# Kernel tuning notes

Hardware: AMD Instinct MI355X
Metric: run time of the kernel (lower is better)

The kernel has to match this reference:

```python
import jax, jax.numpy as jnp
import numpy as np

N_NODES = 50000
N_EDGES = 800000
D_IN = 128
D_HID = 128
N_CLASSES = 40


def gcn_conv(h, src, dst, W, b, n_nodes):
    """GCNConv: out = D^{-1/2} (A + I) D^{-1/2} (h @ W) + b, with self-loops."""
    h = h @ W  # [N, F_out]
    loop = jnp.arange(n_nodes, dtype=src.dtype)
    s = jnp.concatenate([src, loop])  # [E + N]
    d = jnp.concatenate([dst, loop])
    deg = jax.ops.segment_sum(jnp.ones_like(d, dtype=h.dtype), d, num_segments=n_nodes)
    dinv = jax.lax.rsqrt(jnp.maximum(deg, 1.0))  # deg >= 1 due to self-loops
    norm = dinv[s] * dinv[d]  # [E + N]
    msgs = h[s] * norm[:, None]  # gather: [E + N, F_out]
    out = jax.ops.segment_sum(msgs, d, num_segments=n_nodes)  # scatter-add
    return out + b


def setup_inputs() -> dict:
    key = jax.random.key(0)
    ks = jax.random.split(key, 12)
    x = jax.random.normal(ks[0], (N_NODES, D_IN), dtype=jnp.float32)
    edge_index = jax.random.randint(ks[1], (2, N_EDGES), 0, N_NODES, dtype=jnp.int64)
    def lin(k, fi, fo):
        s = 1.0 / np.sqrt(fi)
        return jax.random.uniform(k, (fi, fo), jnp.float32, -s, s)
    W_pre = lin(ks[2], D_IN, D_HID)
    b_pre = jnp.zeros((D_HID,), jnp.float32)
    W1 = lin(ks[3], D_HID, D_HID)
    b1 = jnp.zeros((D_HID,), jnp.float32)
    W2 = lin(ks[4], D_HID, D_HID)
    b2 = jnp.zeros((D_HID,), jnp.float32)
    W_post = lin(ks[5], D_HID, N_CLASSES)
    b_post = jnp.zeros((N_CLASSES,), jnp.float32)
    return {"x": x, "edge_index": edge_index, "W_pre": W_pre, "b_pre": b_pre,
            "W1": W1, "b1": b1, "W2": W2, "b2": b2,
            "W_post": W_post, "b_post": b_post}


def reference(x, edge_index, W_pre, b_pre, W1, b1, W2, b2, W_post, b_post):
    src, dst = edge_index[0], edge_index[1]
    n = x.shape[0]
    h = x @ W_pre + b_pre                      # pre-process MLP (Linear)
    h = jax.nn.relu(gcn_conv(h, src, dst, W1, b1, n))   # conv1 + act1
    h = jax.nn.relu(gcn_conv(h, src, dst, W2, b2, n))   # conv2 + act2
    return h @ W_post + b_post                 # post-process MLP (Linear)
```

## Files before the change

kernel.cpp:

```cpp
#include <hip/hip_runtime.h>

#define D 128

typedef short bfrag __attribute__((ext_vector_type(8)));
typedef float f32x4 __attribute__((ext_vector_type(4)));
typedef unsigned uint32;

__device__ inline unsigned short bf16_rne(float x) {
    unsigned u = __float_as_uint(x);
    return (unsigned short)((u + 0x7FFFu + ((u >> 16) & 1u)) >> 16);
}
__device__ inline float bf16_to_f(unsigned short h) {
    return __uint_as_float(((unsigned)h) << 16);
}
__device__ inline unsigned split2p(float x) {
    unsigned short hi = bf16_rne(x);
    unsigned short lo = bf16_rne(x - bf16_to_f(hi));
    return (unsigned)hi | ((unsigned)lo << 16);
}

__device__ inline void unpair_r(uint4 q0, uint4 q1, bfrag& ah, bfrag& al) {
    union { uint32 u[4]; bfrag b; } H, L;
    H.u[0] = __builtin_amdgcn_perm(q0.y, q0.x, 0x05040100u);
    H.u[1] = __builtin_amdgcn_perm(q0.w, q0.z, 0x05040100u);
    H.u[2] = __builtin_amdgcn_perm(q1.y, q1.x, 0x05040100u);
    H.u[3] = __builtin_amdgcn_perm(q1.w, q1.z, 0x05040100u);
    L.u[0] = __builtin_amdgcn_perm(q0.y, q0.x, 0x07060302u);
    L.u[1] = __builtin_amdgcn_perm(q0.w, q0.z, 0x07060302u);
    L.u[2] = __builtin_amdgcn_perm(q1.y, q1.x, 0x07060302u);
    L.u[3] = __builtin_amdgcn_perm(q1.w, q1.z, 0x07060302u);
    ah = H.b;
    al = L.b;
}

__device__ inline void split8_r(uint4 q0, uint4 q1, bfrag& ah, bfrag& al) {
    float v[8] = {__uint_as_float(q0.x), __uint_as_float(q0.y), __uint_as_float(q0.z), __uint_as_float(q0.w),
                  __uint_as_float(q1.x), __uint_as_float(q1.y), __uint_as_float(q1.z), __uint_as_float(q1.w)};
    union { unsigned short us[8]; bfrag b; } H, L;
    #pragma unroll
    for (int i = 0; i < 8; i++) {
        unsigned pr = split2p(v[i]);
        H.us[i] = (unsigned short)pr;
        L.us[i] = (unsigned short)(pr >> 16);
    }
    ah = H.b;
    al = L.b;
}

__global__ __launch_bounds__(256) void compose_w(const float* __restrict__ Wpre, const float* __restrict__ W1,
                                                 const float* __restrict__ bpre,
                                                 uint32* __restrict__ wcp, float* __restrict__ bc) {
    int gid = blockIdx.x * 256 + threadIdx.x;
    int i = gid >> 2;
    int kq = gid & 3;
    int n = i & 127, k = i >> 7;
    float acc = 0.f;
    #pragma unroll 8
    for (int m = kq * 32; m < kq * 32 + 32; m++)
        acc = fmaf(Wpre[k * 128 + m], W1[m * 128 + n], acc);
    acc += __shfl_xor(acc, 1);
    acc += __shfl_xor(acc, 2);
    if (kq == 0) {
        wcp[n * 128 + k] = split2p(acc);
        if (i < 128) {
            float b = 0.f;
            #pragma unroll 8
            for (int m = 0; m < 128; m++)
                b = fmaf(bpre[m], W1[m * 128 + i], b);
            bc[i] = b;
        }
    }
}

__global__ __launch_bounds__(256) void deg_raw(const unsigned* __restrict__ raw, int* __restrict__ deg,
                                               unsigned* __restrict__ e32, unsigned short* __restrict__ csr16,
                                               float* __restrict__ t_c, int E, int Npad, int csrCap4, int nRows,
                                               const float* __restrict__ W2, const float* __restrict__ Wpost,
                                               uint32* __restrict__ w2_p, uint32* __restrict__ wpost_p) {
    __shared__ int smode;
    int gid = blockIdx.x * 256 + threadIdx.x;
    int gstride = gridDim.x * 256;
    int p0 = blockIdx.x * 1024;
    if (threadIdx.x < 64) {
        int p = p0 + threadIdx.x * 16;
        unsigned v = (p < E) ? raw[2 * p + 1] : 0u;
        unsigned long long any = __ballot(v != 0u);
        if (threadIdx.x == 0) smode = (any != 0ull) ? 1 : 0;
    }
    __syncthreads();
    int m = smode;
    unsigned short sent = (unsigned short)Npad;
    ushort4 s4 = make_ushort4(sent, sent, sent, sent);
    for (int i = gid; i < csrCap4; i += gstride) ((ushort4*)csr16)[i] = s4;
    int sentRows = nRows - Npad;
    int nSentF4 = 8 * sentRows * 4;
    for (int i = gid; i < nSentF4; i += gstride) {
        int chunk = i / (sentRows * 4);
        int rem = i % (sentRows * 4);
        ((float4*)(t_c + (size_t)chunk * nRows * 16 + (size_t)Npad * 16))[rem] = make_float4(0.f, 0.f, 0.f, 0.f);
    }
    for (int i = gid; i < 22528; i += gstride) {
        const float* W; uint32* wp; int idx, ncols;
        if (i < 16384) { W = W2;    wp = w2_p;    idx = i;         ncols = 128; }
        else           { W = Wpost; wp = wpost_p; idx = i - 16384; ncols = 40;  }
        int n = idx >> 7, k = idx & 127;
        float v = (n < ncols) ? W[k * ncols + n] : 0.f;
        wp[idx] = split2p(v);
    }
    int pend = min(p0 + 1024, E);
    for (int p = p0 + threadIdx.x; p < pend; p += 256) {
        int s, d;
        if (m) { s = (int)raw[p]; d = (int)raw[E + p]; }
        else   { s = (int)((const unsigned long long*)raw)[p]; d = (int)((const unsigned long long*)raw)[E + p]; }
        e32[p] = (unsigned)s | ((unsigned)d << 16);
        atomicAdd(&deg[d], 1);
    }
}

__global__ __launch_bounds__(256) void rank_block(const int* __restrict__ deg, float* __restrict__ dinv,
                                                  int* __restrict__ local_rank, int* __restrict__ hist_blk, int N) {
    __shared__ int h[256];
    int t = threadIdx.x;
    h[t] = 0;
    __syncthreads();
    int i = blockIdx.x * 256 + t;
    if (i < N) {
        int d = deg[i];
        dinv[i] = 1.0f / sqrtf((float)(d + 1));
        int b = min(d, 255);
        local_rank[i] = atomicAdd(&h[b], 1);
    }
    __syncthreads();
    hist_blk[blockIdx.x * 256 + t] = h[t];
}

__global__ __launch_bounds__(256) void scan_blocks(int* __restrict__ hist_blk, int* __restrict__ binbase,
                                                   int* __restrict__ ebase, int nblk) {
    int b = threadIdx.x;
    int sum = 0;
    int k = 0;
    for (; k + 8 <= nblk; k += 8) {
        int v[8];
        #pragma unroll
        for (int u = 0; u < 8; u++) v[u] = hist_blk[(k + u) * 256 + b];
        #pragma unroll
        for (int u = 0; u < 8; u++) { hist_blk[(k + u) * 256 + b] = sum; sum += v[u]; }
    }
    for (; k < nblk; k++) {
        int v = hist_blk[k * 256 + b];
        hist_blk[k * 256 + b] = sum;
        sum += v;
    }
    __shared__ int s[256], s2[256];
    int bp = (b + 3) & ~3;
    int c = sum, e = sum * bp;
    s[b] = c; s2[b] = e;
    __syncthreads();
    for (int off = 1; off < 256; off <<= 1) {
        int a0 = (b >= off) ? s[b - off] : 0;
        int a1 = (b >= off) ? s2[b - off] : 0;
        __syncthreads();
        s[b] += a0; s2[b] += a1;
        __syncthreads();
    }
    binbase[b] = s[b] - c;
    ebase[b] = s2[b] - e;
}

__global__ __launch_bounds__(256) void emit_perm(const int* __restrict__ deg, const float* __restrict__ dinv,
                                                 const int* __restrict__ local_rank, const int* __restrict__ hist_blk,
                                                 const int* __restrict__ binbase, const int* __restrict__ ebase,
                                                 int* __restrict__ tailcur, int* __restrict__ rowbeg,
                                                 int* __restrict__ cursor, uint4* __restrict__ meta, int N) {
    int i = blockIdx.x * 256 + threadIdx.x;
    if (i >= N) return;
    int d = deg[i];
    int b = min(d, 255);
    int dp = (d + 3) & ~3;
    int rib = hist_blk[blockIdx.x * 256 + b] + local_rank[i];
    int pos = binbase[b] + rib;
    int rb = (b < 255) ? (ebase[b] + rib * ((b + 3) & ~3)) : (ebase[255] + atomicAdd(tailcur, dp));
    rowbeg[i] = rb;
    cursor[i] = 0;
    meta[pos] = make_uint4((unsigned)rb, (unsigned)dp, __float_as_uint(dinv[i]), (unsigned)i);
}

__global__ __launch_bounds__(256) void fill_csr_32(const unsigned* __restrict__ e32,
                                                   const int* __restrict__ rowbeg, int* __restrict__ cursor,
                                                   unsigned short* __restrict__ csr16, int E) {
    int e = blockIdx.x * 256 + threadIdx.x;
    if (e >= E) return;
    unsigned sd = e32[e];
    int s = (int)(sd & 0xFFFFu), d = (int)(sd >> 16);
    int pos = atomicAdd(&cursor[d], 1);
    csr16[rowbeg[d] + pos] = (unsigned short)s;
}

template<int EPI, int AFMT>
__global__ __launch_bounds__(512) void gemm_lds(const void* __restrict__ Ap,
                                                const uint32* __restrict__ Wpair,
                                                const float* __restrict__ bias,
                                                const float* __restrict__ dinv,
                                                float* __restrict__ Cf,
                                                uint32* __restrict__ Pout,
                                                int nStrips, int N, int nRows) {
    __shared__ uint32 Wl[128 * 132];
    int tid = threadIdx.x;
    for (int i = tid; i < 16384; i += 512)
        Wl[(i >> 7) * 132 + (i & 127)] = Wpair[i];
    __syncthreads();

    int wave = tid >> 6;
    int lane = tid & 63;
    int l15 = lane & 15, lg = lane >> 4;
    int so = wave >> 1;
    int colbase = (wave & 1) * 64;
    size_t chunkStride = (size_t)nRows * 16;

    const int stride = gridDim.x * 4;
    for (int strip = blockIdx.x * 4 + so; strip < nStrips; strip += stride) {
        int arow = min(strip * 16 + l15, N - 1);
        uint4 cur[8];
        const uint4* p = (const uint4*)Ap + (size_t)arow * 32 + lg * 2;
        #pragma unroll
        for (int ks = 0; ks < 4; ks++) {
            cur[2 * ks]     = p[ks * 8];
            cur[2 * ks + 1] = p[ks * 8 + 1];
        }
        bfrag ah[4], al[4];
        #pragma unroll
        for (int ks = 0; ks < 4; ks++) {
            if (AFMT == 0) unpair_r(cur[2 * ks], cur[2 * ks + 1], ah[ks], al[ks]);
            else           split8_r(cur[2 * ks], cur[2 * ks + 1], ah[ks], al[ks]);
        }
        f32x4 acc[4];
        #pragma unroll
        for (int nt = 0; nt < 4; nt++) acc[nt] = (f32x4){0.f, 0.f, 0.f, 0.f};
        #pragma unroll
        for (int ks = 0; ks < 4; ks++) {
            #pragma unroll
            for (int nt = 0; nt < 4; nt++) {
                const uint32* wp = &Wl[(colbase + nt * 16 + l15) * 132 + ks * 32 + lg * 8];
                uint4 w0 = *(const uint4*)wp;
                uint4 w1 = *(const uint4*)(wp + 4);
                bfrag wh, wl_;
                unpair_r(w0, w1, wh, wl_);
                acc[nt] = __builtin_amdgcn_mfma_f32_16x16x32_bf16(ah[ks], wh, acc[nt], 0, 0, 0);
                acc[nt] = __builtin_amdgcn_mfma_f32_16x16x32_bf16(ah[ks], wl_, acc[nt], 0, 0, 0);
                acc[nt] = __builtin_amdgcn_mfma_f32_16x16x32_bf16(al[ks], wh, acc[nt], 0, 0, 0);
            }
        }
        int row0 = strip * 16;
        if (EPI == 0) {
            float dv[4];
            #pragma unroll
            for (int r = 0; r < 4; r++) dv[r] = dinv[min(row0 + lg * 4 + r, N - 1)];
            #pragma unroll
            for (int nt = 0; nt < 4; nt++) {
                int col = colbase + nt * 16 + l15;
                float bv = bias ? bias[col] : 0.f;
                float* cbase = Cf + (size_t)(col >> 4) * chunkStride + (col & 15);
                #pragma unroll
                for (int r = 0; r < 4; r++)
                    cbase[(size_t)(row0 + lg * 4 + r) * 16] = (acc[nt][r] + bv) * dv[r];
            }
        } else {
            #pragma unroll
            for (int nt = 0; nt < 4; nt++) {
                int col = colbase + nt * 16 + l15;
                float bv = bias[col];
                #pragma unroll
                for (int r = 0; r < 4; r++)
                    Pout[(size_t)(row0 + lg * 4 + r) * D + col] = split2p(acc[nt][r] + bv);
            }
        }
    }
}

__global__ __launch_bounds__(256) void gemm_post(const uint32* __restrict__ P,
                                                 const uint32* __restrict__ Wpair,
                                                 const float* __restrict__ bias,
                                                 float* __restrict__ Cf,
                                                 int nStrips, int N, int outW) {
    int wave = threadIdx.x >> 6;
    int lane = threadIdx.x & 63;
    int l15 = lane & 15, lg = lane >> 4;

    bfrag wh[4][3], wl[4][3];
    #pragma unroll
    for (int ks = 0; ks < 4; ks++)
        #pragma unroll
        for (int nt = 0; nt < 3; nt++) {
            const uint32* wp = Wpair + (size_t)(nt * 16 + l15) * D + ks * 32 + lg * 8;
            uint4 w0 = *(const uint4*)wp;
            uint4 w1 = *(const uint4*)(wp + 4);
            unpair_r(w0, w1, wh[ks][nt], wl[ks][nt]);
        }

    const int stride = gridDim.x * 4;
    for (int strip = blockIdx.x * 4 + wave; strip < nStrips; strip += stride) {
        int arow = min(strip * 16 + l15, N - 1);
        bfrag ah[4], al[4];
        #pragma unroll
        for (int ks = 0; ks < 4; ks++) {
            const uint4* p = (const uint4*)P + (size_t)arow * 32 + lg * 2;
            unpair_r(p[ks * 8], p[ks * 8 + 1], ah[ks], al[ks]);
        }
        f32x4 acc[3];
        #pragma unroll
        for (int nt = 0; nt < 3; nt++) acc[nt] = (f32x4){0.f, 0.f, 0.f, 0.f};
        #pragma unroll
        for (int ks = 0; ks < 4; ks++)
            #pragma unroll
            for (int nt = 0; nt < 3; nt++) {
                acc[nt] = __builtin_amdgcn_mfma_f32_16x16x32_bf16(ah[ks], wh[ks][nt], acc[nt], 0, 0, 0);
                acc[nt] = __builtin_amdgcn_mfma_f32_16x16x32_bf16(ah[ks], wl[ks][nt], acc[nt], 0, 0, 0);
                acc[nt] = __builtin_amdgcn_mfma_f32_16x16x32_bf16(al[ks], wh[ks][nt], acc[nt], 0, 0, 0);
            }
        int row0 = strip * 16;
        #pragma unroll
        for (int nt = 0; nt < 3; nt++) {
            int col = nt * 16 + l15;
            #pragma unroll
            for (int r = 0; r < 4; r++) {
                int row = row0 + lg * 4 + r;
                if (row < N && col < outW)
                    Cf[(size_t)row * outW + col] = acc[nt][r] + bias[col];
            }
        }
    }
}

__global__ __launch_bounds__(256) void gather_xcd(const unsigned short* __restrict__ csr16,
                                                  const uint4* __restrict__ meta,
                                                  const float* __restrict__ t_c, const float* __restrict__ bias,
                                                  uint32* __restrict__ Pout, int N, int nRows) {
    int chunk = blockIdx.x & 7;
    int k = (blockIdx.x >> 3) * 16 + (threadIdx.x >> 4);
    if (k >= N) return;
    uint4 m = meta[k];
    int beg = (int)m.x;
    int degp = (int)m.y;
    float di = __uint_as_float(m.z);
    int node = (int)m.w;
    int w = (threadIdx.x >> 2) & 3;
    int c = threadIdx.x & 3;
    const float* tc = t_c + (size_t)chunk * nRows * 16 + c * 4;
    float4 a0 = make_float4(0.f, 0.f, 0.f, 0.f);
    float4 a1 = make_float4(0.f, 0.f, 0.f, 0.f);
    float4 a2 = make_float4(0.f, 0.f, 0.f, 0.f);
    float4 a3 = make_float4(0.f, 0.f, 0.f, 0.f);
    int end = beg + degp;
    for (int j = beg + 4 * w; j < end; j += 16) {
        ushort4 o = *(const ushort4*)(csr16 + j);
        float4 v0 = *(const float4*)(tc + ((size_t)o.x << 4));
        float4 v1 = *(const float4*)(tc + ((size_t)o.y << 4));
        float4 v2 = *(const float4*)(tc + ((size_t)o.z << 4));
        float4 v3 = *(const float4*)(tc + ((size_t)o.w << 4));
        a0.x += v0.x; a0.y += v0.y; a0.z += v0.z; a0.w += v0.w;
        a1.x += v1.x; a1.y += v1.y; a1.z += v1.z; a1.w += v1.w;
        a2.x += v2.x; a2.y += v2.y; a2.z += v2.z; a2.w += v2.w;
        a3.x += v3.x; a3.y += v3.y; a3.z += v3.z; a3.w += v3.w;
    }
    a0.x += a1.x; a0.y += a1.y; a0.z += a1.z; a0.w += a1.w;
    a2.x += a3.x; a2.y += a3.y; a2.z += a3.z; a2.w += a3.w;
    a0.x += a2.x; a0.y += a2.y; a0.z += a2.z; a0.w += a2.w;
    a0.x += __shfl_xor(a0.x, 4); a0.y += __shfl_xor(a0.y, 4);
    a0.z += __shfl_xor(a0.z, 4); a0.w += __shfl_xor(a0.w, 4);
    a0.x += __shfl_xor(a0.x, 8); a0.y += __shfl_xor(a0.y, 8);
    a0.z += __shfl_xor(a0.z, 8); a0.w += __shfl_xor(a0.w, 8);
    if (w != 0) return;
    float4 tv = *(const float4*)(tc + (size_t)node * 16);
    int col0 = chunk * 16 + c * 4;
    float4 b = *((const float4*)bias + (col0 >> 2));
    float4 r;
    r.x = fmaxf(fmaf(di, a0.x + tv.x, b.x), 0.f);
    r.y = fmaxf(fmaf(di, a0.y + tv.y, b.y), 0.f);
    r.z = fmaxf(fmaf(di, a0.z + tv.z, b.z), 0.f);
    r.w = fmaxf(fmaf(di, a0.w + tv.w, b.w), 0.f);
    uint4 p;
    p.x = split2p(r.x); p.y = split2p(r.y); p.z = split2p(r.z); p.w = split2p(r.w);
    *(uint4*)(Pout + (size_t)node * D + col0) = p;
}

extern "C" void kernel_launch(void* const* d_in, const int* in_sizes, int n_in,
                              void* d_out, int out_size, void* d_ws, size_t ws_size,
                              hipStream_t stream) {
    const float* x      = (const float*)d_in[0];
    const unsigned* edges = (const unsigned*)d_in[1];
    const float* W_pre  = (const float*)d_in[2];
    const float* b_pre  = (const float*)d_in[3];
    const float* W1     = (const float*)d_in[4];
    const float* b1     = (const float*)d_in[5];
    const float* W2     = (const float*)d_in[6];
    const float* b2     = (const float*)d_in[7];
    const float* W_post = (const float*)d_in[8];
    const float* b_post = (const float*)d_in[9];
    float* out = (float*)d_out;

    const int N = in_sizes[0] / D;
    const int E = in_sizes[1] / 2;
    const int nStrips = (N + 15) / 16;
    const int Npad = nStrips * 16;
    const int nRows = Npad + 16;
    const int nBlk = (N + 255) / 256;
    const int csrCap = (E + 4 * N + 255) & ~255;

    char* ws = (char*)d_ws;
    size_t off = 0;
    auto alloc = [&](size_t bytes) { void* p = ws + off; off += (bytes + 255) & ~(size_t)255; return p; };
    uint32* pairA = (uint32*)alloc((size_t)Npad * D * 4);
    uint32* pairB = (uint32*)alloc((size_t)Npad * D * 4);
    float*  bufT  = (float*)alloc((size_t)8 * nRows * 16 * 4);
    float*  dinv    = (float*)alloc((size_t)N * 4);
    int*    deg     = (int*)alloc((size_t)N * 4);
    int*    rowbeg  = (int*)alloc((size_t)N * 4);
    unsigned short* csr16 = (unsigned short*)alloc((size_t)csrCap * 2);
    uint4*  meta    = (uint4*)alloc((size_t)N * 16);
    unsigned* e32   = (unsigned*)alloc((size_t)E * 4);
    uint32* wc_p    = (uint32*)alloc(16384 * 4);
    float*  bc      = (float*)alloc(128 * 4);
    uint32* w2_p    = (uint32*)alloc(16384 * 4);
    uint32* wpost_p = (uint32*)alloc(6144 * 4);

    {
        char* t = (char*)bufT;
        size_t toff = 0;
        auto talloc = [&](size_t bytes) { void* p = t + toff; toff += (bytes + 255) & ~(size_t)255; return p; };
        int* cursor     = (int*)talloc((size_t)N * 4);
        int* local_rank = (int*)talloc((size_t)N * 4);
        int* hist_blk   = (int*)talloc((size_t)nBlk * 256 * 4);
        int* mode2      = (int*)talloc(256);
        int* binbase    = (int*)talloc(1024);
        int* ebase      = (int*)talloc(1024);
        int* tailcur = mode2 + 1;

        (void)hipMemsetAsync(mode2, 0, 8, stream);
        (void)hipMemsetAsync(deg, 0, (size_t)N * 4, stream);
        compose_w<<<256, 256, 0, stream>>>(W_pre, W1, b_pre, wc_p, bc);
        deg_raw<<<(E + 1023) / 1024, 256, 0, stream>>>(edges, deg, e32, csr16, bufT, E, Npad, csrCap / 4, nRows,
                                                       W2, W_post, w2_p, wpost_p);
        rank_block<<<nBlk, 256, 0, stream>>>(deg, dinv, local_rank, hist_blk, N);
        scan_blocks<<<1, 256, 0, stream>>>(hist_blk, binbase, ebase, nBlk);
        emit_perm<<<nBlk, 256, 0, stream>>>(deg, dinv, local_rank, hist_blk, binbase, ebase,
                                            tailcur, rowbeg, cursor, meta, N);
        fill_csr_32<<<(E + 255) / 256, 256, 0, stream>>>(e32, rowbeg, cursor, csr16, E);
    }

    const int nGatherBlocks = ((N + 15) / 16) * 8;
    const int gemmGrid = 391;

    gemm_lds<0, 1><<<gemmGrid, 512, 0, stream>>>(x, wc_p, bc, dinv, bufT, nullptr, nStrips, N, nRows);
    gather_xcd<<<nGatherBlocks, 256, 0, stream>>>(csr16, meta, bufT, b1, pairA, N, nRows);

    gemm_lds<0, 0><<<gemmGrid, 512, 0, stream>>>(pairA, w2_p, nullptr, dinv, bufT, nullptr, nStrips, N, nRows);
    gemm_lds<0, 0><<<gemmGrid, 512, 0, stream>>>(pairA, w2_p, nullptr, dinv, bufT, nullptr, nStrips, N, nRows);
    gather_xcd<<<nGatherBlocks, 256, 0, stream>>>(csr16, meta, bufT, b2, pairB, N, nRows);

    gemm_post<<<256, 256, 0, stream>>>(pairB, wpost_p, b_post, out, nStrips, N, 40);
}
```

Baseline: 278.5 us.

## Partition degree count and CSR fill by XCD chunk, fold memsets, drop duplicate GEMM

Splits the degree atomics out of the compaction kernel into a separate kernel that launches eight times as many blocks. Each block handles only edges whose destination falls in the chunk matching blockIdx&7, so that atomics to one destination range land on one XCD's L2. The CSR fill uses the same chunking by row start position. The two memsets move into the compaction kernel, and a duplicated launch of the second-layer GEMM is removed. The cost is reading every edge eight times and launching one extra kernel. The zeroing of deg inside the same grid that never updates it here is safe because counting now happens in a later kernel.

```diff
diff --git a/kernel.cpp b/kernel.cpp
--- a/kernel.cpp
+++ b/kernel.cpp
@@ -72,11 +72,12 @@
     }
 }
 
-__global__ __launch_bounds__(256) void deg_raw(const unsigned* __restrict__ raw, int* __restrict__ deg,
-                                               unsigned* __restrict__ e32, unsigned short* __restrict__ csr16,
-                                               float* __restrict__ t_c, int E, int Npad, int csrCap4, int nRows,
-                                               const float* __restrict__ W2, const float* __restrict__ Wpost,
-                                               uint32* __restrict__ w2_p, uint32* __restrict__ wpost_p) {
+__global__ __launch_bounds__(256) void compact_misc(const unsigned* __restrict__ raw, unsigned* __restrict__ e32,
+                                                    int* __restrict__ deg, int* __restrict__ tailcur,
+                                                    unsigned short* __restrict__ csr16, float* __restrict__ t_c,
+                                                    int E, int N, int Npad, int csrCap4, int nRows,
+                                                    const float* __restrict__ W2, const float* __restrict__ Wpost,
+                                                    uint32* __restrict__ w2_p, uint32* __restrict__ wpost_p) {
     __shared__ int smode;
     int gid = blockIdx.x * 256 + threadIdx.x;
     int gstride = gridDim.x * 256;
@@ -89,6 +90,8 @@
     }
     __syncthreads();
     int m = smode;
+    if (gid == 0) *tailcur = 0;
+    for (int i = gid; i < N; i += gstride) deg[i] = 0;
     unsigned short sent = (unsigned short)Npad;
     ushort4 s4 = make_ushort4(sent, sent, sent, sent);
     for (int i = gid; i < csrCap4; i += gstride) ((ushort4*)csr16)[i] = s4;
@@ -113,8 +116,18 @@
         if (m) { s = (int)raw[p]; d = (int)raw[E + p]; }
         else   { s = (int)((const unsigned long long*)raw)[p]; d = (int)((const unsigned long long*)raw)[E + p]; }
         e32[p] = (unsigned)s | ((unsigned)d << 16);
-        atomicAdd(&deg[d], 1);
-    }
+    }
+}
+
+__global__ __launch_bounds__(256) void deg_count_xcd(const unsigned* __restrict__ e32, int* __restrict__ deg,
+                                                     int E, float scale) {
+    int chunk = blockIdx.x & 7;
+    int e = (blockIdx.x >> 3) * 256 + threadIdx.x;
+    if (e >= E) return;
+    int d = (int)(e32[e] >> 16);
+    int c = min((int)((float)d * scale), 7);
+    if (c != chunk) return;
+    atomicAdd(&deg[d], 1);
 }
 
 __global__ __launch_bounds__(256) void rank_block(const int* __restrict__ deg, float* __restrict__ dinv,
@@ -185,15 +198,19 @@
     meta[pos] = make_uint4((unsigned)rb, (unsigned)dp, __float_as_uint(dinv[i]), (unsigned)i);
 }
 
-__global__ __launch_bounds__(256) void fill_csr_32(const unsigned* __restrict__ e32,
-                                                   const int* __restrict__ rowbeg, int* __restrict__ cursor,
-                                                   unsigned short* __restrict__ csr16, int E) {
-    int e = blockIdx.x * 256 + threadIdx.x;
+__global__ __launch_bounds__(256) void fill_csr_xcd(const unsigned* __restrict__ e32, const int* __restrict__ rowbeg,
+                                                    int* __restrict__ cursor, unsigned short* __restrict__ csr16,
+                                                    int E, float scale) {
+    int chunk = blockIdx.x & 7;
+    int e = (blockIdx.x >> 3) * 256 + threadIdx.x;
     if (e >= E) return;
     unsigned sd = e32[e];
-    int s = (int)(sd & 0xFFFFu), d = (int)(sd >> 16);
+    int d = (int)(sd >> 16);
+    int rb = rowbeg[d];
+    int c = min((int)((float)rb * scale), 7);
+    if (c != chunk) return;
     int pos = atomicAdd(&cursor[d], 1);
-    csr16[rowbeg[d] + pos] = (unsigned short)s;
+    csr16[rb + pos] = (unsigned short)(sd & 0xFFFFu);
 }
 
 template<int EPI, int AFMT>
@@ -435,16 +452,20 @@
         int* ebase      = (int*)talloc(1024);
         int* tailcur = mode2 + 1;
 
-        (void)hipMemsetAsync(mode2, 0, 8, stream);
-        (void)hipMemsetAsync(deg, 0, (size_t)N * 4, stream);
+        const float scaleDeg  = 8.0f / (float)N;
+        const float scaleFill = 8.0f / (float)csrCap;
+        const int nEdgeBlk8 = ((E + 255) / 256) * 8;
+
         compose_w<<<256, 256, 0, stream>>>(W_pre, W1, b_pre, wc_p, bc);
-        deg_raw<<<(E + 1023) / 1024, 256, 0, stream>>>(edges, deg, e32, csr16, bufT, E, Npad, csrCap / 4, nRows,
-                                                       W2, W_post, w2_p, wpost_p);
+        compact_misc<<<(E + 1023) / 1024, 256, 0, stream>>>(edges, e32, deg, tailcur, csr16, bufT,
+                                                            E, N, Npad, csrCap / 4, nRows,
+                                                            W2, W_post, w2_p, wpost_p);
+        deg_count_xcd<<<nEdgeBlk8, 256, 0, stream>>>(e32, deg, E, scaleDeg);
         rank_block<<<nBlk, 256, 0, stream>>>(deg, dinv, local_rank, hist_blk, N);
         scan_blocks<<<1, 256, 0, stream>>>(hist_blk, binbase, ebase, nBlk);
         emit_perm<<<nBlk, 256, 0, stream>>>(deg, dinv, local_rank, hist_blk, binbase, ebase,
                                             tailcur, rowbeg, cursor, meta, N);
-        fill_csr_32<<<(E + 255) / 256, 256, 0, stream>>>(e32, rowbeg, cursor, csr16, E);
+        fill_csr_xcd<<<nEdgeBlk8, 256, 0, stream>>>(e32, rowbeg, cursor, csr16, E, scaleFill);
     }
 
     const int nGatherBlocks = ((N + 15) / 16) * 8;
@@ -454,7 +475,6 @@
     gather_xcd<<<nGatherBlocks, 256, 0, stream>>>(csr16, meta, bufT, b1, pairA, N, nRows);
 
     gemm_lds<0, 0><<<gemmGrid, 512, 0, stream>>>(pairA, w2_p, nullptr, dinv, bufT, nullptr, nStrips, N, nRows);
-    gemm_lds<0, 0><<<gemmGrid, 512, 0, stream>>>(pairA, w2_p, nullptr, dinv, bufT, nullptr, nStrips, N, nRows);
     gather_xcd<<<nGatherBlocks, 256, 0, stream>>>(csr16, meta, bufT, b2, pairB, N, nRows);
 
     gemm_post<<<256, 256, 0, stream>>>(pairB, wpost_p, b_post, out, nStrips, N, 40);
```

Result: faster. 257.3 us (median of 3 runs) (-7.6%).
